# Optimization experiments

Hardware: AMD Instinct MI355X
Metric: run time of the kernel (lower is better)

The kernel has to match this reference:

```python
import jax, jax.numpy as jnp
import numpy as np

NEG_INF = -1e12  # stanza's constant.INFINITY_NUMBER


def setup_inputs() -> dict:
    key = jax.random.key(0)
    k1, k2, k3, k4, k5, k6 = jax.random.split(key, 6)
    B, S, D = 128, 8192, 128
    inp = jax.random.normal(k1, (B, D), dtype=jnp.float32)
    context = jax.random.normal(k2, (B, S, D), dtype=jnp.float32)
    mask = jax.random.bernoulli(k3, 0.3, (B, S))  # True = masked out
    # learned params (torch nn.Linear convention: y = x @ W.T)
    W = jax.random.normal(k4, (D, D), dtype=jnp.float32) / np.sqrt(D)
    V = jax.random.normal(k5, (1, D), dtype=jnp.float32) / np.sqrt(D)
    Wout = jax.random.normal(k6, (D, 2 * D), dtype=jnp.float32) / np.sqrt(2 * D)
    return {"input": inp, "context": context, "mask": mask, "W": W, "V": V, "Wout": Wout}


def reference(input, context, mask, W, V, Wout):
    # u = ReLU(W x): per-batch, identical across source positions -> compute once
    u = jax.nn.relu(jnp.einsum('bd,ed->be', input, W))          # [B, D]
    v = jax.nn.relu(jnp.einsum('bsd,ed->bse', context, W))      # [B, S, D]
    # a = V . (u o v)
    attn = jnp.einsum('be,bse,e->bs', u, v, V[0])               # [B, S]
    attn = jnp.where(mask, NEG_INF, attn)
    attn = jax.nn.softmax(attn, axis=1)
    weighted = jnp.einsum('bs,bsd->bd', attn, context)          # [B, D]
    h_tilde = jnp.tanh(jnp.einsum('bf,ef->be', jnp.concatenate([weighted, input], axis=1), Wout))
    return (h_tilde, attn)
```

## Files before the change

kernel.cpp:

```cpp
#include <hip/hip_runtime.h>


#define BB 128
#define SS 8192
#define DD 128

typedef float f32x4_t __attribute__((ext_vector_type(4)));
typedef short bf16x8_t __attribute__((ext_vector_type(8)));
typedef unsigned short u16x8_t __attribute__((ext_vector_type(8)));
typedef unsigned int u32x4_t __attribute__((ext_vector_type(4)));
typedef int i32x4_t __attribute__((ext_vector_type(4)));

__device__ __forceinline__ unsigned short f2bf(float x) {
  unsigned u = __builtin_bit_cast(unsigned, x);
  unsigned r = (u + 0x7FFFu + ((u >> 16) & 1u)) >> 16;
  return (unsigned short)r;
}
__device__ __forceinline__ float bf2f(unsigned short h) {
  unsigned u = ((unsigned)h) << 16;
  return __builtin_bit_cast(float, u);
}
__device__ __forceinline__ unsigned cvtpk(float a, float b) {
  unsigned r;
  asm("v_cvt_pk_bf16_f32 %0, %1, %2" : "=v"(r) : "v"(a), "v"(b));
  return r;
}

__global__ void k_detect(const unsigned int* __restrict__ mw, unsigned int* __restrict__ flag) {
  int i = blockIdx.x * 256 + threadIdx.x;
  unsigned v = mw[i];
  unsigned f = 0;
  if (v == 0x3F800000u) f = 2u;
  else if (v > 1u) f = 1u;
  if (f) atomicOr(flag, f);
}

__global__ void k_prep(const float* __restrict__ inp, const float* __restrict__ Wg,
                       const float* __restrict__ Vg, unsigned short* __restrict__ Whi,
                       unsigned short* __restrict__ Wlo, float* __restrict__ wv) {
  const int b = blockIdx.x, tid = threadIdx.x;
  {
    int i = b * DD + tid;
    float x = Wg[i];
    unsigned short h = f2bf(x);
    Whi[i] = h;
    Wlo[i] = f2bf(x - bf2f(h));
  }
  __shared__ float xin[DD];
  xin[tid] = inp[b * DD + tid];
  __syncthreads();
  const float* wr = Wg + tid * DD;
  float s = 0.f;
#pragma unroll 8
  for (int d = 0; d < DD; ++d) s += xin[d] * wr[d];
  wv[b * DD + tid] = fmaxf(s, 0.f) * Vg[tid];
}

__launch_bounds__(512, 1)
__global__ void k_logits(const float* __restrict__ ctx, const unsigned short* __restrict__ Whi,
                         const unsigned short* __restrict__ Wlo, const float* __restrict__ wv,
                         const void* __restrict__ maskp, const unsigned int* __restrict__ flag,
                         float* __restrict__ logits, float* __restrict__ Wslice,
                         float* __restrict__ stats) {
  __shared__ unsigned short WPKH[16384];
  __shared__ unsigned short WPKL[16384];
  __shared__ float wl[DD];
  __shared__ float WB[8][DD];
  __shared__ float MS[8][2];

  const int tid = threadIdx.x;
  const int b = blockIdx.y;
  const int slice = blockIdx.x;
  const int wave = tid >> 6;
  const int lane = tid & 63;
  const int lr = lane & 15;
  const int lg = lane >> 4;
  const unsigned mode = *flag;

  const long rowb0 = (long)b * SS + (long)slice * 2048 + (long)wave * 256;

  f32x4_t xA[8], xB[8];
  auto issue = [&](f32x4_t (&x)[8], long grow, int rt) {
    const float* rp = ctx + (grow + rt * 16 + lr) * (long)DD + lg * 8;
#pragma unroll
    for (int ks = 0; ks < 4; ++ks) {
      x[ks * 2]     = *(const f32x4_t*)(rp + ks * 32);
      x[ks * 2 + 1] = *(const f32x4_t*)(rp + ks * 32 + 4);
    }
  };

  issue(xA, rowb0, 0);

#pragma unroll
  for (int jj = 0; jj < 4; ++jj) {
    int p = tid + jj * 512;
    int frag = p >> 6;
    int li = p & 63;
    int et = frag >> 2, ks = frag & 3;
    int lg2 = li >> 4, lr2 = li & 15;
    int src = (et * 16 + lr2) * DD + ks * 32 + lg2 * 8;
    *(u16x8_t*)(&WPKH[p * 8]) = *(const u16x8_t*)(&Whi[src]);
    *(u16x8_t*)(&WPKL[p * 8]) = *(const u16x8_t*)(&Wlo[src]);
  }
  if (tid < DD) wl[tid] = wv[b * DD + tid];
  __syncthreads();

  float wfreg[8];
#pragma unroll
  for (int et = 0; et < 8; ++et) wfreg[et] = wl[et * 16 + lr];

  float m_run = -3.4e38f, s_run = 0.f;
  f32x4_t wacc[8];
#pragma unroll
  for (int k = 0; k < 8; ++k) wacc[k] = f32x4_t{0.f, 0.f, 0.f, 0.f};

  auto process = [&](const f32x4_t (&x)[8], long grow, int rt) {
    bf16x8_t a[4];
#pragma unroll
    for (int ks = 0; ks < 4; ++ks) {
      u32x4_t hh;
      hh[0] = cvtpk(x[ks * 2][0], x[ks * 2][1]);
      hh[1] = cvtpk(x[ks * 2][2], x[ks * 2][3]);
      hh[2] = cvtpk(x[ks * 2 + 1][0], x[ks * 2 + 1][1]);
      hh[3] = cvtpk(x[ks * 2 + 1][2], x[ks * 2 + 1][3]);
      a[ks] = __builtin_bit_cast(bf16x8_t, hh);
    }
    f32x4_t part = {0.f, 0.f, 0.f, 0.f};
#pragma unroll
    for (int et = 0; et < 8; ++et) {
      f32x4_t v1 = {0.f, 0.f, 0.f, 0.f};
      f32x4_t v2 = v1;
#pragma unroll
      for (int ks = 0; ks < 4; ++ks) {
        const int pidx = ((((et << 2) | ks) << 6) | lane) << 3;
        bf16x8_t bh = *(const bf16x8_t*)(&WPKH[pidx]);
        bf16x8_t bl = *(const bf16x8_t*)(&WPKL[pidx]);
        v1 = __builtin_amdgcn_mfma_f32_16x16x32_bf16(a[ks], bh, v1, 0, 0, 0);
        v2 = __builtin_amdgcn_mfma_f32_16x16x32_bf16(a[ks], bl, v2, 0, 0, 0);
      }
      const float wf = wfreg[et];
#pragma unroll
      for (int i = 0; i < 4; ++i)
        part[i] += wf * fmaxf(v1[i] + v2[i], 0.f);
    }
#pragma unroll
    for (int m2 = 1; m2 < 16; m2 <<= 1) {
      part[0] += __shfl_xor(part[0], m2, 64);
      part[1] += __shfl_xor(part[1], m2, 64);
      part[2] += __shfl_xor(part[2], m2, 64);
      part[3] += __shfl_xor(part[3], m2, 64);
    }
    const long rowb = grow + rt * 16 + lg * 4;
    bool mk0, mk1, mk2, mk3;
    if (mode == 0) {
      i32x4_t mv = *(const i32x4_t*)((const int*)maskp + rowb);
      mk0 = mv[0] != 0; mk1 = mv[1] != 0; mk2 = mv[2] != 0; mk3 = mv[3] != 0;
    } else if (mode == 1) {
      unsigned mb = *(const unsigned*)((const unsigned char*)maskp + rowb);
      mk0 = (mb & 255u) != 0; mk1 = ((mb >> 8) & 255u) != 0;
      mk2 = ((mb >> 16) & 255u) != 0; mk3 = (mb >> 24) != 0;
    } else {
      f32x4_t mf = *(const f32x4_t*)((const float*)maskp + rowb);
      mk0 = mf[0] != 0.f; mk1 = mf[1] != 0.f; mk2 = mf[2] != 0.f; mk3 = mf[3] != 0.f;
    }
    part[0] = mk0 ? -1e12f : part[0];
    part[1] = mk1 ? -1e12f : part[1];
    part[2] = mk2 ? -1e12f : part[2];
    part[3] = mk3 ? -1e12f : part[3];
    if (lr == 0) *(f32x4_t*)(&logits[rowb]) = part;
    float gm = fmaxf(fmaxf(part[0], part[1]), fmaxf(part[2], part[3]));
    gm = fmaxf(gm, __shfl_xor(gm, 16, 64));
    gm = fmaxf(gm, __shfl_xor(gm, 32, 64));
    if (gm > m_run) {
      float sc = expf(m_run - gm);
      s_run *= sc;
#pragma unroll
      for (int k = 0; k < 8; ++k) {
        wacc[k][0] *= sc; wacc[k][1] *= sc; wacc[k][2] *= sc; wacc[k][3] *= sc;
      }
      m_run = gm;
    }
    float pv0 = expf(part[0] - m_run);
    float pv1 = expf(part[1] - m_run);
    float pv2 = expf(part[2] - m_run);
    float pv3 = expf(part[3] - m_run);
    s_run += (pv0 + pv1) + (pv2 + pv3);
    const int srcl = (lane & 12) << 2;
    float q0 = __shfl(pv0, srcl, 64);
    float q1 = __shfl(pv1, srcl, 64);
    float q2 = __shfl(pv2, srcl, 64);
    float q3 = __shfl(pv3, srcl, 64);
    const int sel = lane & 3;
    float pn = sel == 0 ? q0 : sel == 1 ? q1 : sel == 2 ? q2 : q3;
#pragma unroll
    for (int k = 0; k < 8; ++k) {
      wacc[k][0] += pn * x[k][0]; wacc[k][1] += pn * x[k][1];
      wacc[k][2] += pn * x[k][2]; wacc[k][3] += pn * x[k][3];
    }
  };

#pragma unroll 1
  for (int g = 0; g < 8; ++g) {
    const long grow = rowb0 + (long)g * 32;
    issue(xB, grow, 1);
    process(xA, grow, 0);
    if (g < 7) issue(xA, grow + 32, 0);
    process(xB, grow, 1);
  }

#pragma unroll
  for (int m2 = 1; m2 < 16; m2 <<= 1) {
#pragma unroll
    for (int k = 0; k < 8; ++k) {
      wacc[k][0] += __shfl_xor(wacc[k][0], m2, 64);
      wacc[k][1] += __shfl_xor(wacc[k][1], m2, 64);
      wacc[k][2] += __shfl_xor(wacc[k][2], m2, 64);
      wacc[k][3] += __shfl_xor(wacc[k][3], m2, 64);
    }
  }
  float st = s_run;
  st += __shfl_xor(st, 16, 64);
  st += __shfl_xor(st, 32, 64);
  if (lr == 0) {
#pragma unroll
    for (int k = 0; k < 8; ++k) {
      int ks = k >> 1, half = k & 1;
      int col = ks * 32 + lg * 8 + half * 4;
      WB[wave][col + 0] = wacc[k][0];
      WB[wave][col + 1] = wacc[k][1];
      WB[wave][col + 2] = wacc[k][2];
      WB[wave][col + 3] = wacc[k][3];
    }
  }
  if (lane == 0) { MS[wave][0] = m_run; MS[wave][1] = st; }
  __syncthreads();
  if (tid < DD) {
    float M = MS[0][0];
#pragma unroll
    for (int w = 1; w < 8; ++w) M = fmaxf(M, MS[w][0]);
    float Wv = 0.f, S = 0.f;
#pragma unroll
    for (int w = 0; w < 8; ++w) {
      float e = expf(MS[w][0] - M);
      Wv += WB[w][tid] * e;
      S  += MS[w][1] * e;
    }
    Wslice[(long)(b * 4 + slice) * DD + tid] = Wv;
    if (tid == 0) {
      stats[(b * 4 + slice) * 2 + 0] = M;
      stats[(b * 4 + slice) * 2 + 1] = S;
    }
  }
}

__global__ void k_attn(float* attnbuf, const float* __restrict__ stats) {
  const int b = blockIdx.x, c = blockIdx.y;
  const int tid = threadIdx.x;
  float m0 = stats[b * 8 + 0], s0 = stats[b * 8 + 1];
  float m1 = stats[b * 8 + 2], s1 = stats[b * 8 + 3];
  float m2 = stats[b * 8 + 4], s2 = stats[b * 8 + 5];
  float m3 = stats[b * 8 + 6], s3 = stats[b * 8 + 7];
  float M = fmaxf(fmaxf(m0, m1), fmaxf(m2, m3));
  float S = s0 * expf(m0 - M) + s1 * expf(m1 - M) + s2 * expf(m2 - M) + s3 * expf(m3 - M);
  float inv = 1.f / S;
  const long off = (long)b * SS + (long)c * 2048 + (long)tid * 4;
  f32x4_t v = *(const f32x4_t*)(attnbuf + off);
  v[0] = expf(v[0] - M) * inv;
  v[1] = expf(v[1] - M) * inv;
  v[2] = expf(v[2] - M) * inv;
  v[3] = expf(v[3] - M) * inv;
  *(f32x4_t*)(attnbuf + off) = v;
}

__global__ void k_final(const float* __restrict__ Wslice, const float* __restrict__ stats,
                        const float* __restrict__ inp, const float* __restrict__ Wout,
                        float* __restrict__ hout) {
  const int b = blockIdx.x;
  const int tid = threadIdx.x;
  __shared__ float wsh[DD], xin[DD];
  float m0 = stats[b * 8 + 0], s0 = stats[b * 8 + 1];
  float m1 = stats[b * 8 + 2], s1 = stats[b * 8 + 3];
  float m2 = stats[b * 8 + 4], s2 = stats[b * 8 + 5];
  float m3 = stats[b * 8 + 6], s3 = stats[b * 8 + 7];
  float M = fmaxf(fmaxf(m0, m1), fmaxf(m2, m3));
  float e0 = expf(m0 - M), e1 = expf(m1 - M), e2 = expf(m2 - M), e3 = expf(m3 - M);
  float S = s0 * e0 + s1 * e1 + s2 * e2 + s3 * e3;
  float Wv = Wslice[(long)(b * 4 + 0) * DD + tid] * e0
           + Wslice[(long)(b * 4 + 1) * DD + tid] * e1
           + Wslice[(long)(b * 4 + 2) * DD + tid] * e2
           + Wslice[(long)(b * 4 + 3) * DD + tid] * e3;
  wsh[tid] = Wv / S;
  xin[tid] = inp[b * DD + tid];
  __syncthreads();
  const float* wr = Wout + tid * (2 * DD);
  float s = 0.f;
#pragma unroll 8
  for (int f = 0; f < DD; ++f) s += wsh[f] * wr[f];
#pragma unroll 8
  for (int f = 0; f < DD; ++f) s += xin[f] * wr[DD + f];
  hout[b * DD + tid] = tanhf(s);
}

extern "C" void kernel_launch(void* const* d_in, const int* in_sizes, int n_in,
                              void* d_out, int out_size, void* d_ws, size_t ws_size,
                              hipStream_t stream) {
  const float* inp  = (const float*)d_in[0];
  const float* ctx  = (const float*)d_in[1];
  const void*  mask = d_in[2];
  const float* Wg   = (const float*)d_in[3];
  const float* Vg   = (const float*)d_in[4];
  const float* Wout = (const float*)d_in[5];

  float* out = (float*)d_out;
  float* h_out = out;
  float* attn_out = out + BB * DD;

  char* ws = (char*)d_ws;
  unsigned int*   flag   = (unsigned int*)ws;
  unsigned short* Whi    = (unsigned short*)(ws + 1024);
  unsigned short* Wlo    = (unsigned short*)(ws + 1024 + 32768);
  float*          wv     = (float*)(ws + 1024 + 65536);
  float*          Wslice = (float*)(ws + 1024 + 65536 + 65536);
  float*          stats  = (float*)(ws + 1024 + 65536 + 65536 + 262144);

  (void)hipMemsetAsync(flag, 0, 4, stream);
  k_detect<<<dim3(256),   dim3(256), 0, stream>>>((const unsigned int*)mask, flag);
  k_prep  <<<dim3(BB),    dim3(DD),  0, stream>>>(inp, Wg, Vg, Whi, Wlo, wv);
  k_logits<<<dim3(4, BB), dim3(512), 0, stream>>>(ctx, Whi, Wlo, wv, mask, flag,
                                                  attn_out, Wslice, stats);
  k_attn  <<<dim3(BB, 4), dim3(512), 0, stream>>>(attn_out, stats);
  k_final <<<dim3(BB),    dim3(128), 0, stream>>>(Wslice, stats, inp, Wout, h_out);
}
```

Measured before the change: 167.2 us.

## Process two row tiles per iteration, sharing W fragment loads and bf16 context

```diff
diff --git a/kernel.cpp b/kernel.cpp
--- a/kernel.cpp
+++ b/kernel.cpp
@@ -79,17 +79,20 @@
 
   const long rowb0 = (long)b * SS + (long)slice * 2048 + (long)wave * 256;
 
-  f32x4_t xA[8], xB[8];
-  auto issue = [&](f32x4_t (&x)[8], long grow, int rt) {
-    const float* rp = ctx + (grow + rt * 16 + lr) * (long)DD + lg * 8;
-#pragma unroll
-    for (int ks = 0; ks < 4; ++ks) {
-      x[ks * 2]     = *(const f32x4_t*)(rp + ks * 32);
-      x[ks * 2 + 1] = *(const f32x4_t*)(rp + ks * 32 + 4);
+  f32x4_t xbuf[16];
+  auto issue = [&](long grow) {
+#pragma unroll
+    for (int rt = 0; rt < 2; ++rt) {
+      const float* rp = ctx + (grow + rt * 16 + lr) * (long)DD + lg * 8;
+#pragma unroll
+      for (int ks = 0; ks < 4; ++ks) {
+        xbuf[rt * 8 + ks * 2]     = *(const f32x4_t*)(rp + ks * 32);
+        xbuf[rt * 8 + ks * 2 + 1] = *(const f32x4_t*)(rp + ks * 32 + 4);
+      }
     }
   };
 
-  issue(xA, rowb0, 0);
+  issue(rowb0);
 
 #pragma unroll
   for (int jj = 0; jj < 4; ++jj) {
@@ -114,61 +117,84 @@
 #pragma unroll
   for (int k = 0; k < 8; ++k) wacc[k] = f32x4_t{0.f, 0.f, 0.f, 0.f};
 
-  auto process = [&](const f32x4_t (&x)[8], long grow, int rt) {
-    bf16x8_t a[4];
-#pragma unroll
-    for (int ks = 0; ks < 4; ++ks) {
-      u32x4_t hh;
-      hh[0] = cvtpk(x[ks * 2][0], x[ks * 2][1]);
-      hh[1] = cvtpk(x[ks * 2][2], x[ks * 2][3]);
-      hh[2] = cvtpk(x[ks * 2 + 1][0], x[ks * 2 + 1][1]);
-      hh[3] = cvtpk(x[ks * 2 + 1][2], x[ks * 2 + 1][3]);
-      a[ks] = __builtin_bit_cast(bf16x8_t, hh);
-    }
-    f32x4_t part = {0.f, 0.f, 0.f, 0.f};
+#pragma unroll 1
+  for (int g = 0; g < 8; ++g) {
+    const long grow = rowb0 + (long)g * 32;
+    bf16x8_t a[2][4];
+#pragma unroll
+    for (int rt = 0; rt < 2; ++rt) {
+#pragma unroll
+      for (int ks = 0; ks < 4; ++ks) {
+        f32x4_t x0 = xbuf[rt * 8 + ks * 2];
+        f32x4_t x1 = xbuf[rt * 8 + ks * 2 + 1];
+        u32x4_t hh;
+        hh[0] = cvtpk(x0[0], x0[1]);
+        hh[1] = cvtpk(x0[2], x0[3]);
+        hh[2] = cvtpk(x1[0], x1[1]);
+        hh[3] = cvtpk(x1[2], x1[3]);
+        a[rt][ks] = __builtin_bit_cast(bf16x8_t, hh);
+      }
+    }
+    if (g < 7) issue(grow + 32);
+
+    f32x4_t part[2] = {{0.f, 0.f, 0.f, 0.f}, {0.f, 0.f, 0.f, 0.f}};
 #pragma unroll
     for (int et = 0; et < 8; ++et) {
-      f32x4_t v1 = {0.f, 0.f, 0.f, 0.f};
-      f32x4_t v2 = v1;
+      bf16x8_t bh[4], bl[4];
 #pragma unroll
       for (int ks = 0; ks < 4; ++ks) {
         const int pidx = ((((et << 2) | ks) << 6) | lane) << 3;
-        bf16x8_t bh = *(const bf16x8_t*)(&WPKH[pidx]);
-        bf16x8_t bl = *(const bf16x8_t*)(&WPKL[pidx]);
-        v1 = __builtin_amdgcn_mfma_f32_16x16x32_bf16(a[ks], bh, v1, 0, 0, 0);
-        v2 = __builtin_amdgcn_mfma_f32_16x16x32_bf16(a[ks], bl, v2, 0, 0, 0);
+        bh[ks] = *(const bf16x8_t*)(&WPKH[pidx]);
+        bl[ks] = *(const bf16x8_t*)(&WPKL[pidx]);
       }
       const float wf = wfreg[et];
 #pragma unroll
-      for (int i = 0; i < 4; ++i)
-        part[i] += wf * fmaxf(v1[i] + v2[i], 0.f);
-    }
-#pragma unroll
-    for (int m2 = 1; m2 < 16; m2 <<= 1) {
-      part[0] += __shfl_xor(part[0], m2, 64);
-      part[1] += __shfl_xor(part[1], m2, 64);
-      part[2] += __shfl_xor(part[2], m2, 64);
-      part[3] += __shfl_xor(part[3], m2, 64);
-    }
-    const long rowb = grow + rt * 16 + lg * 4;
-    bool mk0, mk1, mk2, mk3;
-    if (mode == 0) {
-      i32x4_t mv = *(const i32x4_t*)((const int*)maskp + rowb);
-      mk0 = mv[0] != 0; mk1 = mv[1] != 0; mk2 = mv[2] != 0; mk3 = mv[3] != 0;
-    } else if (mode == 1) {
-      unsigned mb = *(const unsigned*)((const unsigned char*)maskp + rowb);
-      mk0 = (mb & 255u) != 0; mk1 = ((mb >> 8) & 255u) != 0;
-      mk2 = ((mb >> 16) & 255u) != 0; mk3 = (mb >> 24) != 0;
-    } else {
-      f32x4_t mf = *(const f32x4_t*)((const float*)maskp + rowb);
-      mk0 = mf[0] != 0.f; mk1 = mf[1] != 0.f; mk2 = mf[2] != 0.f; mk3 = mf[3] != 0.f;
-    }
-    part[0] = mk0 ? -1e12f : part[0];
-    part[1] = mk1 ? -1e12f : part[1];
-    part[2] = mk2 ? -1e12f : part[2];
-    part[3] = mk3 ? -1e12f : part[3];
-    if (lr == 0) *(f32x4_t*)(&logits[rowb]) = part;
-    float gm = fmaxf(fmaxf(part[0], part[1]), fmaxf(part[2], part[3]));
+      for (int rt = 0; rt < 2; ++rt) {
+        f32x4_t v1 = {0.f, 0.f, 0.f, 0.f};
+        f32x4_t v2 = v1;
+#pragma unroll
+        for (int ks = 0; ks < 4; ++ks) {
+          v1 = __builtin_amdgcn_mfma_f32_16x16x32_bf16(a[rt][ks], bh[ks], v1, 0, 0, 0);
+          v2 = __builtin_amdgcn_mfma_f32_16x16x32_bf16(a[rt][ks], bl[ks], v2, 0, 0, 0);
+        }
+#pragma unroll
+        for (int i = 0; i < 4; ++i)
+          part[rt][i] += wf * fmaxf(v1[i] + v2[i], 0.f);
+      }
+    }
+#pragma unroll
+    for (int rt = 0; rt < 2; ++rt) {
+#pragma unroll
+      for (int m2 = 1; m2 < 16; m2 <<= 1) {
+        part[rt][0] += __shfl_xor(part[rt][0], m2, 64);
+        part[rt][1] += __shfl_xor(part[rt][1], m2, 64);
+        part[rt][2] += __shfl_xor(part[rt][2], m2, 64);
+        part[rt][3] += __shfl_xor(part[rt][3], m2, 64);
+      }
+    }
+#pragma unroll
+    for (int rt = 0; rt < 2; ++rt) {
+      const long rowb = grow + rt * 16 + lg * 4;
+      bool mk0, mk1, mk2, mk3;
+      if (mode == 0) {
+        i32x4_t mv = *(const i32x4_t*)((const int*)maskp + rowb);
+        mk0 = mv[0] != 0; mk1 = mv[1] != 0; mk2 = mv[2] != 0; mk3 = mv[3] != 0;
+      } else if (mode == 1) {
+        unsigned mb = *(const unsigned*)((const unsigned char*)maskp + rowb);
+        mk0 = (mb & 255u) != 0; mk1 = ((mb >> 8) & 255u) != 0;
+        mk2 = ((mb >> 16) & 255u) != 0; mk3 = (mb >> 24) != 0;
+      } else {
+        f32x4_t mf = *(const f32x4_t*)((const float*)maskp + rowb);
+        mk0 = mf[0] != 0.f; mk1 = mf[1] != 0.f; mk2 = mf[2] != 0.f; mk3 = mf[3] != 0.f;
+      }
+      part[rt][0] = mk0 ? -1e12f : part[rt][0];
+      part[rt][1] = mk1 ? -1e12f : part[rt][1];
+      part[rt][2] = mk2 ? -1e12f : part[rt][2];
+      part[rt][3] = mk3 ? -1e12f : part[rt][3];
+      if (lr == 0) *(f32x4_t*)(&logits[rowb]) = part[rt];
+    }
+    float gm = fmaxf(fmaxf(fmaxf(part[0][0], part[0][1]), fmaxf(part[0][2], part[0][3])),
+                     fmaxf(fmaxf(part[1][0], part[1][1]), fmaxf(part[1][2], part[1][3])));
     gm = fmaxf(gm, __shfl_xor(gm, 16, 64));
     gm = fmaxf(gm, __shfl_xor(gm, 32, 64));
     if (gm > m_run) {
@@ -180,32 +206,32 @@
       }
       m_run = gm;
     }
-    float pv0 = expf(part[0] - m_run);
-    float pv1 = expf(part[1] - m_run);
-    float pv2 = expf(part[2] - m_run);
-    float pv3 = expf(part[3] - m_run);
-    s_run += (pv0 + pv1) + (pv2 + pv3);
     const int srcl = (lane & 12) << 2;
-    float q0 = __shfl(pv0, srcl, 64);
-    float q1 = __shfl(pv1, srcl, 64);
-    float q2 = __shfl(pv2, srcl, 64);
-    float q3 = __shfl(pv3, srcl, 64);
     const int sel = lane & 3;
-    float pn = sel == 0 ? q0 : sel == 1 ? q1 : sel == 2 ? q2 : q3;
-#pragma unroll
-    for (int k = 0; k < 8; ++k) {
-      wacc[k][0] += pn * x[k][0]; wacc[k][1] += pn * x[k][1];
-      wacc[k][2] += pn * x[k][2]; wacc[k][3] += pn * x[k][3];
-    }
-  };
-
-#pragma unroll 1
-  for (int g = 0; g < 8; ++g) {
-    const long grow = rowb0 + (long)g * 32;
-    issue(xB, grow, 1);
-    process(xA, grow, 0);
-    if (g < 7) issue(xA, grow + 32, 0);
-    process(xB, grow, 1);
+#pragma unroll
+    for (int rt = 0; rt < 2; ++rt) {
+      float pv0 = expf(part[rt][0] - m_run);
+      float pv1 = expf(part[rt][1] - m_run);
+      float pv2 = expf(part[rt][2] - m_run);
+      float pv3 = expf(part[rt][3] - m_run);
+      s_run += (pv0 + pv1) + (pv2 + pv3);
+      float q0 = __shfl(pv0, srcl, 64);
+      float q1 = __shfl(pv1, srcl, 64);
+      float q2 = __shfl(pv2, srcl, 64);
+      float q3 = __shfl(pv3, srcl, 64);
+      float pn = sel == 0 ? q0 : sel == 1 ? q1 : sel == 2 ? q2 : q3;
+#pragma unroll
+      for (int ks = 0; ks < 4; ++ks) {
+        u32x4_t u = __builtin_bit_cast(u32x4_t, a[rt][ks]);
+#pragma unroll
+        for (int j = 0; j < 4; ++j) {
+          float flo = __builtin_bit_cast(float, u[j] << 16);
+          float fhi = __builtin_bit_cast(float, u[j] & 0xFFFF0000u);
+          wacc[ks * 2 + (j >> 1)][(j & 1) * 2 + 0] += pn * flo;
+          wacc[ks * 2 + (j >> 1)][(j & 1) * 2 + 1] += pn * fhi;
+        }
+      }
+    }
   }
 
 #pragma unroll
```

New measurement: 165.0 us. Within noise of the previous version (-1.3%).
